# Kernel optimization log

Hardware: AMD Instinct MI355X
Metric: run time of the kernel (lower is better)

The kernel has to match this reference:

```python
import jax, jax.numpy as jnp
import numpy as np

N = 50000
E = 1600000
HID = 128
H = 8
D = HID // H


def _layer_norm(x, g, b, eps=1e-5):
    mu = jnp.mean(x, axis=-1, keepdims=True)
    var = jnp.mean(jnp.square(x - mu), axis=-1, keepdims=True)
    return (x - mu) * jax.lax.rsqrt(var + eps) * g + b


def setup_inputs() -> dict:
    key = jax.random.key(0)
    ks = jax.random.split(key, 20)
    s = 1.0 / np.sqrt(HID)
    inp = {
        "x": jax.random.normal(ks[0], (N, HID), jnp.float32),
        "edge_index": jax.random.randint(ks[1], (2, E), 0, N, jnp.int64),
        "edge_attr": jax.random.randint(ks[2], (E,), 0, 13, jnp.int64),
        # projections (stored as [in, out] so y = x @ W + b)
        "Wq": jax.random.normal(ks[3], (HID, HID), jnp.float32) * s,
        "bq": jnp.zeros((HID,), jnp.float32),
        "Wk": jax.random.normal(ks[4], (HID, HID), jnp.float32) * s,
        "bk": jnp.zeros((HID,), jnp.float32),
        "Wv": jax.random.normal(ks[5], (HID, HID), jnp.float32) * s,
        "bv": jnp.zeros((HID,), jnp.float32),
        "Wo": jax.random.normal(ks[6], (HID, HID), jnp.float32) * s,
        "bo": jnp.zeros((HID,), jnp.float32),
        "edge_bias_table": jax.random.normal(ks[7], (13, H), jnp.float32) * 0.02,
        "W1": jax.random.normal(ks[8], (HID, 4 * HID), jnp.float32) * s,
        "b1": jnp.zeros((4 * HID,), jnp.float32),
        "W2": jax.random.normal(ks[9], (4 * HID, HID), jnp.float32) * (0.5 * s),
        "b2": jnp.zeros((HID,), jnp.float32),
        "g1": jnp.ones((HID,), jnp.float32),
        "be1": jnp.zeros((HID,), jnp.float32),
        "g2": jnp.ones((HID,), jnp.float32),
        "be2": jnp.zeros((HID,), jnp.float32),
    }
    return inp


def reference(x, edge_index, edge_attr, Wq, bq, Wk, bk, Wv, bv, Wo, bo,
              edge_bias_table, W1, b1, W2, b2, g1, be1, g2, be2):
    n = x.shape[0]
    residual = x
    h = _layer_norm(x, g1, be1)
    Q = (h @ Wq + bq).reshape(n, H, D)
    K = (h @ Wk + bk).reshape(n, H, D)
    V = (h @ Wv + bv).reshape(n, H, D)
    src, dst = edge_index[0], edge_index[1]
    # per-edge scores [E, H]
    scores = jnp.sum(Q[dst] * K[src], axis=-1) / np.sqrt(D)
    scores = scores + edge_bias_table[jnp.clip(edge_attr, 0, 12)]
    # scatter softmax over incoming edges of each dst (global max, as in source)
    scores_exp = jnp.exp(scores - jnp.max(scores))
    attn_sum = jax.ops.segment_sum(scores_exp, dst, num_segments=n)  # [N, H]
    attn_w = scores_exp / (attn_sum[dst] + 1e-8)                      # [E, H]
    messages = V[src] * attn_w[..., None]                             # [E, H, D]
    out = jax.ops.segment_sum(messages, dst, num_segments=n)          # [N, H, D]
    out = out.reshape(n, HID) @ Wo + bo
    x = residual + out  # dropout is identity in eval
    residual = x
    h2 = _layer_norm(x, g2, be2)
    ffn = jax.nn.relu(h2 @ W1 + b1) @ W2 + b2
    return residual + ffn
```

## Files before the change

### kernel.cpp

```cpp
#include <hip/hip_runtime.h>
#include <hip/hip_bf16.h>

#define N_NODES 50000
#define E_EDGES 1600000
#define HID 128
#define NH 8
#define HD 16

#define NBKT 196
#define BKT_CAP 9216
#define CHUNK_A 4096
#define EPT 16
#define BINA_BLOCKS ((E_EDGES + CHUNK_A - 1) / CHUNK_A)
#define WCVT_BLOCKS 771
#define LN_BLOCKS 12500
#define QKV_XBLOCKS ((N_NODES + 127) / 128)
#define ATTN_BLOCKS 2048

using short8 = __attribute__((ext_vector_type(8))) short;
using f32x4  = __attribute__((ext_vector_type(4))) float;
using f32x2  = __attribute__((ext_vector_type(2))) float;
typedef _Float16 h16x2 __attribute__((ext_vector_type(2)));

#if defined(__has_builtin) && __has_builtin(__builtin_amdgcn_fdot2)
#define FDOT2(a, b, c) __builtin_amdgcn_fdot2((a), (b), (c), false)
#else
__device__ __forceinline__ float FDOT2(h16x2 a, h16x2 b, float c) {
    return fmaf((float)a[0], (float)b[0], fmaf((float)a[1], (float)b[1], c));
}
#endif

__device__ __forceinline__ float wave_reduce_sum(float v) {
    #pragma unroll
    for (int off = 32; off > 0; off >>= 1) v += __shfl_xor(v, off, 64);
    return v;
}

__device__ __forceinline__ unsigned int packbf2(float a, float b) {
    __hip_bfloat162 t;
    t.x = __float2bfloat16(a);
    t.y = __float2bfloat16(b);
    unsigned int u;
    __builtin_memcpy(&u, &t, 4);
    return u;
}

__device__ __forceinline__ unsigned short bf16u(float v) {
    __hip_bfloat16 t = __float2bfloat16(v);
    unsigned short u;
    __builtin_memcpy(&u, &t, 2);
    return u;
}

__device__ __forceinline__ unsigned char fp8e(float v) {
    return (unsigned char)(__builtin_amdgcn_cvt_pk_fp8_f32(v, v, 0u, false) & 0xFFu);
}

union U4H {
    uint4 u;
    h16x2 h[4];
};

struct KV {
    U4H k0, k1;
    uint4 v;
};

__device__ __forceinline__ KV loadkv(const char* khs, const unsigned char* v8s, unsigned pk) {
    KV r;
    unsigned rr = pk & 0xFFFFu;
    r.k0.u = *(const uint4*)(khs + (rr << 8));
    r.k1.u = *(const uint4*)(khs + (rr << 8) + 16u);
    r.v = *(const uint4*)(v8s + (rr << 7));
    return r;
}

__device__ __forceinline__ void consume_kv(const KV& kv, unsigned pk, bool vd,
                                           const U4H& q0, const U4H& q1,
                                           const float* bLDS, int sub,
                                           f32x2* acc2, float& wsum) {
    float p = 0.f;
    #pragma unroll
    for (int j = 0; j < 4; ++j) p = FDOT2(q0.h[j], kv.k0.h[j], p);
    #pragma unroll
    for (int j = 0; j < 4; ++j) p = FDOT2(q1.h[j], kv.k1.h[j], p);
    float s = p + bLDS[((pk >> 16) & 0xFu) * 8 + sub];
    float w = vd ? __expf(s) : 0.f;
    wsum += w;
    f32x2 w2; w2[0] = w; w2[1] = w;
    f32x2 t;
    t = __builtin_amdgcn_cvt_pk_f32_fp8(kv.v.x, false); acc2[0] = t * w2 + acc2[0];
    t = __builtin_amdgcn_cvt_pk_f32_fp8(kv.v.x, true);  acc2[1] = t * w2 + acc2[1];
    t = __builtin_amdgcn_cvt_pk_f32_fp8(kv.v.y, false); acc2[2] = t * w2 + acc2[2];
    t = __builtin_amdgcn_cvt_pk_f32_fp8(kv.v.y, true);  acc2[3] = t * w2 + acc2[3];
    t = __builtin_amdgcn_cvt_pk_f32_fp8(kv.v.z, false); acc2[4] = t * w2 + acc2[4];
    t = __builtin_amdgcn_cvt_pk_f32_fp8(kv.v.z, true);  acc2[5] = t * w2 + acc2[5];
    t = __builtin_amdgcn_cvt_pk_f32_fp8(kv.v.w, false); acc2[6] = t * w2 + acc2[6];
    t = __builtin_amdgcn_cvt_pk_f32_fp8(kv.v.w, true);  acc2[7] = t * w2 + acc2[7];
}

__global__ __launch_bounds__(256) void prep_kernel(
    const int* __restrict__ ei, const int* __restrict__ attr,
    int* __restrict__ bcur, unsigned int* __restrict__ temp,
    const float* __restrict__ Wq, const float* __restrict__ Wk,
    const float* __restrict__ Wv, const float* __restrict__ Wo,
    const float* __restrict__ W1, const float* __restrict__ W2,
    const float* __restrict__ bq, const float* __restrict__ bk,
    const float* __restrict__ bv,
    __hip_bfloat16* __restrict__ Wqkvt, __hip_bfloat16* __restrict__ Wot,
    __hip_bfloat16* __restrict__ W1t, __hip_bfloat16* __restrict__ W2t,
    float* __restrict__ bqkv,
    const float* __restrict__ x, const float* __restrict__ g1,
    const float* __restrict__ be1, __hip_bfloat16* __restrict__ h_out) {
    __shared__ unsigned int sval[CHUNK_A];
    __shared__ unsigned short sbkt[CHUNK_A];
    __shared__ int hist[NBKT];
    __shared__ int lofs[NBKT];
    __shared__ int gbase[NBKT];
    __shared__ int lcur[NBKT];
    __shared__ int sc[256];
    const int b = blockIdx.x;
    const int tid = threadIdx.x;
    if (b < BINA_BLOCKS) {
        const int e0 = b * CHUNK_A;
        const int n = min(CHUNK_A, E_EDGES - e0);
        for (int i = tid; i < NBKT; i += 256) hist[i] = 0;
        __syncthreads();
        unsigned int v[EPT];
        short bk_[EPT];
        #pragma unroll
        for (int j = 0; j < EPT; ++j) {
            int i = tid + j * 256;
            bk_[j] = -1;
            v[j] = 0;
            if (i < n) {
                int e = e0 + i;
                int src = ei[e];
                int dst = ei[E_EDGES + e];
                int a = attr[e]; a = min(max(a, 0), 12);
                v[j] = (unsigned)src | ((unsigned)a << 16) | ((unsigned)(dst & 255) << 20);
                int bb = dst >> 8;
                bk_[j] = (short)bb;
                atomicAdd(&hist[bb], 1);
            }
        }
        __syncthreads();
        sc[tid] = (tid < NBKT) ? hist[tid] : 0;
        __syncthreads();
        for (int off = 1; off < 256; off <<= 1) {
            int xx = (tid >= off) ? sc[tid - off] : 0;
            __syncthreads();
            sc[tid] += xx;
            __syncthreads();
        }
        if (tid < NBKT) {
            int h = hist[tid];
            lofs[tid] = sc[tid] - h;
            lcur[tid] = 0;
            gbase[tid] = h ? atomicAdd(&bcur[tid], h) : 0;
        }
        __syncthreads();
        #pragma unroll
        for (int j = 0; j < EPT; ++j) {
            if (bk_[j] >= 0) {
                int p = lofs[bk_[j]] + atomicAdd(&lcur[bk_[j]], 1);
                sval[p] = v[j];
                sbkt[p] = (unsigned short)bk_[j];
            }
        }
        __syncthreads();
        for (int i = tid; i < n; i += 256) {
            int bb = sbkt[i];
            temp[(size_t)bb * BKT_CAP + gbase[bb] + (i - lofs[bb])] = sval[i];
        }
    } else if (b < BINA_BLOCKS + WCVT_BLOCKS) {
        int t = (b - BINA_BLOCKS) * 256 + tid;
        if (t >= 196608) {
            int i = t - 196608;
            if (i < 384) bqkv[i] = i < 128 ? bq[i] : (i < 256 ? bk[i - 128] : bv[i - 256]);
            return;
        }
        const float* W; __hip_bfloat16* Wt; int K, N, idx;
        if (t < 65536) {
            int which = t >> 14; idx = t & 16383; K = 128; N = 128;
            W = which == 0 ? Wq : which == 1 ? Wk : which == 2 ? Wv : Wo;
            Wt = which == 3 ? Wot : Wqkvt + which * 16384;
        } else if (t < 131072) { idx = t - 65536;  K = 128; N = 512; W = W1; Wt = W1t; }
        else                   { idx = t - 131072; K = 512; N = 128; W = W2; Wt = W2t; }
        int n = idx / K, k = idx - n * K;
        Wt[idx] = __float2bfloat16(W[(size_t)k * N + n]);
    } else {
        int wave = tid >> 6;
        int lane = tid & 63;
        int row = (b - BINA_BLOCKS - WCVT_BLOCKS) * 4 + wave;
        if (row >= N_NODES) return;
        float2 v = ((const float2*)(x + (size_t)row * HID))[lane];
        float s = wave_reduce_sum(v.x + v.y);
        float mu = s * (1.0f / HID);
        float dx = v.x - mu, dy = v.y - mu;
        float q = wave_reduce_sum(dx * dx + dy * dy);
        float rstd = rsqrtf(q * (1.0f / HID) + 1e-5f);
        float2 gg = ((const float2*)g1)[lane];
        float2 bb = ((const float2*)be1)[lane];
        __hip_bfloat162 o;
        o.x = __float2bfloat16(dx * rstd * gg.x + bb.x);
        o.y = __float2bfloat16(dy * rstd * gg.y + bb.y);
        ((__hip_bfloat162*)(h_out + (size_t)row * HID))[lane] = o;
    }
}

__global__ __launch_bounds__(512) void qkv_binb_kernel(
    const int* __restrict__ bcur, const unsigned int* __restrict__ temp,
    unsigned int* __restrict__ packed, int* __restrict__ offs,
    const __hip_bfloat16* __restrict__ A, const __hip_bfloat16* __restrict__ Wt,
    const float* __restrict__ bias,
    _Float16* __restrict__ Chh, unsigned char* __restrict__ C8, int M) {
    __shared__ short8 smem[2048 + 2048];
    const int tid = threadIdx.x;
    if (blockIdx.x < NBKT) {
        int* cnts = (int*)smem;
        int* hist = cnts + 256;
        int* cur = hist + 256;
        const int b = blockIdx.x;
        if (tid < 256) {
            cnts[tid] = (tid < NBKT) ? bcur[tid] : 0;
            hist[tid] = 0;
        }
        __syncthreads();
        for (int off = 1; off < 256; off <<= 1) {
            int x = 0;
            if (tid < 256 && tid >= off) x = cnts[tid - off];
            __syncthreads();
            if (tid < 256) cnts[tid] += x;
            __syncthreads();
        }
        const int cnt = bcur[b];
        const int start = cnts[b] - cnt;
        const size_t base = (size_t)b * BKT_CAP;
        for (int i = tid; i < cnt; i += 512)
            atomicAdd(&hist[(temp[base + i] >> 20) & 255], 1);
        __syncthreads();
        if (tid < 256) cur[tid] = hist[tid];
        __syncthreads();
        for (int off = 1; off < 256; off <<= 1) {
            int x = 0;
            if (tid < 256 && tid >= off) x = cur[tid - off];
            __syncthreads();
            if (tid < 256) cur[tid] += x;
            __syncthreads();
        }
        const int node0 = b * 256;
        if (tid < 256) {
            int excl = cur[tid] - hist[tid];
            cur[tid] = excl;
            int node = node0 + tid;
            if (node < N_NODES) offs[node] = start + excl;
        }
        if (b == NBKT - 1 && tid == 0) offs[N_NODES] = start + cnt;
        __syncthreads();
        for (int i = tid; i < cnt; i += 512) {
            unsigned int v = temp[base + i];
            int d = (v >> 20) & 255;
            int p = start + atomicAdd(&cur[d], 1);
            packed[p] = v & 0xFFFFFu;
        }
        return;
    }
    const int gb = blockIdx.x - NBKT;
    const int plane = gb / QKV_XBLOCKS;
    const int xb = gb - plane * QKV_XBLOCKS;
    const int row0 = xb * 128;
    const int col0 = plane * 128;
    const int w = tid >> 6, l = tid & 63;
    const int lr = l & 15, hi = l >> 4;
    f32x4 acc[8] = {};
    #pragma unroll
    for (int it = 0; it < 4; ++it) {
        unsigned d = tid + it * 512;
        int r = d >> 4, sd = d & 15;
        int ss = sd ^ (r & 7);
        int gr = row0 + r; if (gr >= M) gr = M - 1;
        __builtin_amdgcn_global_load_lds(
            (const __attribute__((address_space(1))) void*)(A + (size_t)gr * 128 + ss * 8),
            (__attribute__((address_space(3))) void*)(smem + (d & ~63u)),
            16, 0, 0);
    }
    #pragma unroll
    for (int it = 0; it < 4; ++it) {
        unsigned d = tid + it * 512;
        int r = d >> 4, sd = d & 15;
        int ss = sd ^ (r & 7);
        __builtin_amdgcn_global_load_lds(
            (const __attribute__((address_space(1))) void*)(Wt + (size_t)(col0 + r) * 128 + ss * 8),
            (__attribute__((address_space(3))) void*)(smem + 2048 + (d & ~63u)),
            16, 0, 0);
    }
    __syncthreads();
    const int ar = w * 16 + lr;
    #pragma unroll
    for (int ks = 0; ks < 4; ++ks) {
        int s = ks * 4 + hi;
        short8 a = smem[ar * 16 + (s ^ (ar & 7))];
        #pragma unroll
        for (int f = 0; f < 8; ++f) {
            int br = f * 16 + lr;
            short8 b = smem[2048 + br * 16 + (s ^ (br & 7))];
            acc[f] = __builtin_amdgcn_mfma_f32_16x16x32_bf16(a, b, acc[f], 0, 0, 0);
        }
    }
    const float scl = (plane == 0) ? 0.25f : 1.0f;
    #pragma unroll
    for (int f = 0; f < 8; ++f) {
        int c = col0 + f * 16 + lr;
        float bv = bias[c];
        #pragma unroll
        for (int j = 0; j < 4; ++j) {
            int r = row0 + w * 16 + hi * 4 + j;
            if (r < M) {
                float v = acc[f][j] + bv;
                if (plane < 2)
                    Chh[(size_t)plane * N_NODES * 128 + (size_t)r * 128 + (c & 127)] =
                        (_Float16)(v * scl);
                else
                    C8[(size_t)r * 128 + (c & 127)] = fp8e(v);
            }
        }
    }
}

__global__ __launch_bounds__(256) void tail_kernel(
    const __hip_bfloat16* __restrict__ attn_ob,
    const __hip_bfloat16* __restrict__ Wot,
    const float* __restrict__ bo,
    const float* __restrict__ x,
    const float* __restrict__ g2, const float* __restrict__ be2,
    const __hip_bfloat16* __restrict__ W1t,
    const float* __restrict__ b1,
    const __hip_bfloat16* __restrict__ W2t,
    const float* __restrict__ b2,
    float* __restrict__ outp, int M) {
    __shared__ short8 hseg[32 * 16];
    __shared__ short8 wseg[2048];
    __shared__ short8 bseg[1024];
    __shared__ float lnS[2][32];
    __shared__ float lnQ[2][32];
    const int tid = threadIdx.x;
    const int row0 = blockIdx.x * 32;
    const int w = tid >> 6, l = tid & 63;
    const int lr = l & 15, hi = l >> 4;
    const int rt = w & 1, ch = w >> 1;
    #pragma unroll
    for (int it = 0; it < 2; ++it) {
        unsigned d = tid + it * 256;
        int r = d >> 4, sd = d & 15;
        int ss = sd ^ (r & 7);
        int gr = row0 + r; if (gr >= M) gr = M - 1;
        __builtin_amdgcn_global_load_lds(
            (const __attribute__((address_space(1))) void*)(attn_ob + (size_t)gr * 128 + ss * 8),
            (__attribute__((address_space(3))) void*)(hseg + (d & ~63u)),
            16, 0, 0);
    }
    #pragma unroll
    for (int it = 0; it < 8; ++it) {
        unsigned d = tid + it * 256;
        int r = d >> 4, sd = d & 15;
        int ss = sd ^ (r & 7);
        __builtin_amdgcn_global_load_lds(
            (const __attribute__((address_space(1))) void*)(Wot + (size_t)r * 128 + ss * 8),
            (__attribute__((address_space(3))) void*)(wseg + (d & ~63u)),
            16, 0, 0);
    }
    __syncthreads();
    const int ar = rt * 16 + lr;
    f32x4 acc[4] = {};
    #pragma unroll
    for (int ks = 0; ks < 4; ++ks) {
        int s = ks * 4 + hi;
        short8 a = hseg[ar * 16 + (s ^ (ar & 7))];
        #pragma unroll
        for (int f = 0; f < 4; ++f) {
            int br = ch * 64 + f * 16 + lr;
            short8 b = wseg[br * 16 + (s ^ (br & 7))];
            acc[f] = __builtin_amdgcn_mfma_f32_16x16x32_bf16(a, b, acc[f], 0, 0, 0);
        }
    }
    float vv[4][4];
    float gc[4], bc[4];
    #pragma unroll
    for (int f = 0; f < 4; ++f) {
        int c = ch * 64 + f * 16 + lr;
        gc[f] = g2[c]; bc[f] = be2[c];
        float bv = bo[c];
        #pragma unroll
        for (int j = 0; j < 4; ++j) {
            int r = row0 + rt * 16 + hi * 4 + j;
            int rr = r < M ? r : M - 1;
            vv[f][j] = acc[f][j] + bv + x[(size_t)rr * 128 + c];
        }
    }
    float ps[4], pq[4];
    #pragma unroll
    for (int j = 0; j < 4; ++j) {
        float s = 0.f, q = 0.f;
        #pragma unroll
        for (int f = 0; f < 4; ++f) { s += vv[f][j]; q += vv[f][j] * vv[f][j]; }
        #pragma unroll
        for (int m = 1; m <= 8; m <<= 1) { s += __shfl_xor(s, m); q += __shfl_xor(q, m); }
        ps[j] = s; pq[j] = q;
    }
    if (lr == 0) {
        #pragma unroll
        for (int j = 0; j < 4; ++j) {
            int r = rt * 16 + hi * 4 + j;
            lnS[ch][r] = ps[j];
            lnQ[ch][r] = pq[j];
        }
    }
    __syncthreads();
    unsigned short* hu = (unsigned short*)hseg;
    #pragma unroll
    for (int j = 0; j < 4; ++j) {
        int r = rt * 16 + hi * 4 + j;
        float s = lnS[0][r] + lnS[1][r];
        float q = lnQ[0][r] + lnQ[1][r];
        float mu = s * (1.0f / 128.0f);
        float rstd = rsqrtf(q * (1.0f / 128.0f) - mu * mu + 1e-5f);
        #pragma unroll
        for (int f = 0; f < 4; ++f) {
            int c = ch * 64 + f * 16 + lr;
            int seg = c >> 3;
            float hv = (vv[f][j] - mu) * rstd * gc[f] + bc[f];
            hu[r * 128 + ((seg ^ (r & 7)) << 3) + (c & 7)] = bf16u(hv);
        }
    }
    __syncthreads();
    unsigned short* f1u = (unsigned short*)wseg;
    for (int cc = 0; cc < 8; ++cc) {
        #pragma unroll
        for (int it = 0; it < 4; ++it) {
            unsigned d = tid + it * 256;
            int rb = d >> 4, sd = d & 15;
            int ss = sd ^ (rb & 7);
            __builtin_amdgcn_global_load_lds(
                (const __attribute__((address_space(1))) void*)(W1t + (size_t)(cc * 64 + rb) * 128 + ss * 8),
                (__attribute__((address_space(3))) void*)(bseg + (d & ~63u)),
                16, 0, 0);
        }
        __syncthreads();
        f32x4 a0 = {}, a1 = {};
        #pragma unroll
        for (int ks = 0; ks < 4; ++ks) {
            int s = ks * 4 + hi;
            short8 a = hseg[ar * 16 + (s ^ (ar & 7))];
            int rb0 = ch * 32 + lr;
            short8 b0 = bseg[rb0 * 16 + (s ^ (rb0 & 7))];
            a0 = __builtin_amdgcn_mfma_f32_16x16x32_bf16(a, b0, a0, 0, 0, 0);
            int rb1 = ch * 32 + 16 + lr;
            short8 b1v = bseg[rb1 * 16 + (s ^ (rb1 & 7))];
            a1 = __builtin_amdgcn_mfma_f32_16x16x32_bf16(a, b1v, a1, 0, 0, 0);
        }
        #pragma unroll
        for (int f = 0; f < 2; ++f) {
            int c = cc * 64 + ch * 32 + f * 16 + lr;
            float bv = b1[c];
            int seg = c >> 3;
            #pragma unroll
            for (int j = 0; j < 4; ++j) {
                int r = rt * 16 + hi * 4 + j;
                float v = fmaxf((f == 0 ? a0[j] : a1[j]) + bv, 0.f);
                f1u[r * 512 + ((seg ^ (r & 7)) << 3) + (c & 7)] = bf16u(v);
            }
        }
        __syncthreads();
    }
    f32x4 acc2[4] = {};
    for (int kc = 0; kc < 8; ++kc) {
        #pragma unroll
        for (int it = 0; it < 4; ++it) {
            unsigned d = tid + it * 256;
            int rb = d >> 3, sd = d & 7;
            int ss = sd ^ (rb & 7);
            __builtin_amdgcn_global_load_lds(
                (const __attribute__((address_space(1))) void*)(W2t + (size_t)rb * 512 + kc * 64 + ss * 8),
                (__attribute__((address_space(3))) void*)(bseg + (d & ~63u)),
                16, 0, 0);
        }
        __syncthreads();
        #pragma unroll
        for (int ks = 0; ks < 2; ++ks) {
            int ksg = kc * 8 + ks * 4 + hi;
            short8 a = *(const short8*)&f1u[ar * 512 + ((ksg ^ (ar & 7)) << 3)];
            int s2 = ks * 4 + hi;
            #pragma unroll
            for (int f = 0; f < 4; ++f) {
                int rb = ch * 64 + f * 16 + lr;
                short8 b = bseg[rb * 8 + (s2 ^ (rb & 7))];
                acc2[f] = __builtin_amdgcn_mfma_f32_16x16x32_bf16(a, b, acc2[f], 0, 0, 0);
            }
        }
        __syncthreads();
    }
    #pragma unroll
    for (int f = 0; f < 4; ++f) {
        int c = ch * 64 + f * 16 + lr;
        float bv = b2[c];
        #pragma unroll
        for (int j = 0; j < 4; ++j) {
            int r = row0 + rt * 16 + hi * 4 + j;
            if (r < M)
                outp[(size_t)r * 128 + c] = acc2[f][j] + bv + vv[f][j];
        }
    }
}

__global__ __launch_bounds__(256) void fused_attn_kernel(
    const unsigned int* __restrict__ packed,
    const int* __restrict__ offs,
    const _Float16* __restrict__ qkh,
    const unsigned char* __restrict__ v8p,
    const float* __restrict__ btab,
    __hip_bfloat16* __restrict__ out) {
    __shared__ float bLDS[104];
    const int tid = threadIdx.x;
    if (tid < 104) bLDS[tid] = btab[tid];
    __syncthreads();
    const int wave = tid >> 6, lane = tid & 63;
    const int slot = lane >> 3, sub = lane & 7;
    const char* qh = (const char*)qkh;
    const unsigned sb = (unsigned)sub << 5;
    const char* khs = (const char*)(qkh + (size_t)N_NODES * 128) + sb;
    const unsigned char* v8s = v8p + (sb >> 1);
    const unsigned gwave = blockIdx.x * 4 + wave;
    const unsigned stride = ATTN_BLOCKS * 4;
    for (unsigned n = gwave; n < N_NODES; n += stride) {
        U4H q0, q1;
        q0.u = *(const uint4*)(qh + (n << 8) + sb);
        q1.u = *(const uint4*)(qh + (n << 8) + sb + 16u);
        const int lo = offs[n], hi = offs[n + 1];
        const int nit = (hi - lo + 7) >> 3;
        f32x2 acc2[8] = {};
        float wsum = 0.f;
        int i = lo + slot;
        bool vd0 = i < hi;       unsigned pk0 = vd0 ? packed[i] : 0u;
        bool vd1 = i + 8 < hi;   unsigned pk1 = vd1 ? packed[i + 8] : 0u;
        KV a = loadkv(khs, v8s, pk0);
        KV b = loadkv(khs, v8s, pk1);
        int ii = i + 16;
        int rem = nit;
        while (rem >= 2) {
            const bool vd2 = ii < hi;
            const unsigned pk2 = vd2 ? packed[ii] : 0u;
            const bool vd3 = ii + 8 < hi;
            const unsigned pk3 = vd3 ? packed[ii + 8] : 0u;
            consume_kv(a, pk0, vd0, q0, q1, bLDS, sub, acc2, wsum);
            a = loadkv(khs, v8s, pk2);
            consume_kv(b, pk1, vd1, q0, q1, bLDS, sub, acc2, wsum);
            b = loadkv(khs, v8s, pk3);
            pk0 = pk2; vd0 = vd2;
            pk1 = pk3; vd1 = vd3;
            ii += 16;
            rem -= 2;
        }
        if (rem == 1) consume_kv(a, pk0, vd0, q0, q1, bLDS, sub, acc2, wsum);
        float accf[16];
        #pragma unroll
        for (int j = 0; j < 8; ++j) { accf[2 * j] = acc2[j][0]; accf[2 * j + 1] = acc2[j][1]; }
        #pragma unroll
        for (int j = 0; j < 16; ++j) {
            accf[j] += __shfl_xor(accf[j], 8);
            accf[j] += __shfl_xor(accf[j], 16);
            accf[j] += __shfl_xor(accf[j], 32);
        }
        wsum += __shfl_xor(wsum, 8);
        wsum += __shfl_xor(wsum, 16);
        wsum += __shfl_xor(wsum, 32);
        if (slot == 0) {
            float inv = 1.0f / (wsum + 1e-8f);
            uint4 o0, o1;
            o0.x = packbf2(accf[0] * inv, accf[1] * inv);
            o0.y = packbf2(accf[2] * inv, accf[3] * inv);
            o0.z = packbf2(accf[4] * inv, accf[5] * inv);
            o0.w = packbf2(accf[6] * inv, accf[7] * inv);
            o1.x = packbf2(accf[8] * inv, accf[9] * inv);
            o1.y = packbf2(accf[10] * inv, accf[11] * inv);
            o1.z = packbf2(accf[12] * inv, accf[13] * inv);
            o1.w = packbf2(accf[14] * inv, accf[15] * inv);
            char* op = (char*)out + (n << 8) + ((unsigned)sub << 5);
            *(uint4*)op = o0;
            *(uint4*)(op + 16) = o1;
        }
    }
}

extern "C" void kernel_launch(void* const* d_in, const int* in_sizes, int n_in,
                              void* d_out, int out_size, void* d_ws, size_t ws_size,
                              hipStream_t stream) {
    const float* x    = (const float*)d_in[0];
    const int*   ei   = (const int*)d_in[1];
    const int*   attr = (const int*)d_in[2];
    const float* Wq   = (const float*)d_in[3];
    const float* bq   = (const float*)d_in[4];
    const float* Wk   = (const float*)d_in[5];
    const float* bk   = (const float*)d_in[6];
    const float* Wv   = (const float*)d_in[7];
    const float* bv   = (const float*)d_in[8];
    const float* Wo   = (const float*)d_in[9];
    const float* bo   = (const float*)d_in[10];
    const float* ebt  = (const float*)d_in[11];
    const float* W1   = (const float*)d_in[12];
    const float* b1   = (const float*)d_in[13];
    const float* W2   = (const float*)d_in[14];
    const float* b2   = (const float*)d_in[15];
    const float* g1   = (const float*)d_in[16];
    const float* be1  = (const float*)d_in[17];
    const float* g2   = (const float*)d_in[18];
    const float* be2  = (const float*)d_in[19];
    float* out = (float*)d_out;

    char* ws = (char*)d_ws;
    const size_t szRowB = (size_t)N_NODES * HID * 2;
    const size_t ALIGN = 256;
    #define ALN(v) (((v) + ALIGN - 1) & ~(ALIGN - 1))
    size_t o = 0;
    __hip_bfloat16* h_buf = (__hip_bfloat16*)(ws + o); o += szRowB;
    _Float16* QKh = (_Float16*)(ws + o); o += (size_t)N_NODES * 256 * 2;
    unsigned char* V8 = (unsigned char*)(ws + o); o += (size_t)N_NODES * 128;
    unsigned int* packed = (unsigned int*)(ws + o); o += (size_t)E_EDGES * 4;
    unsigned int* temp = (unsigned int*)(ws + o); o += (size_t)NBKT * BKT_CAP * 4;
    int* bcur = (int*)(ws + o); o = ALN(o + (size_t)NBKT * 4);
    int* offs = (int*)(ws + o); o = ALN(o + (size_t)(N_NODES + 1) * 4);
    __hip_bfloat16* attn_ob = (__hip_bfloat16*)(ws + o); o += szRowB;
    __hip_bfloat16* Wqkvt = (__hip_bfloat16*)(ws + o); o += 384 * 128 * 2;
    __hip_bfloat16* Wot = (__hip_bfloat16*)(ws + o); o += 128 * 128 * 2;
    __hip_bfloat16* W1t = (__hip_bfloat16*)(ws + o); o += 512 * 128 * 2;
    __hip_bfloat16* W2t = (__hip_bfloat16*)(ws + o); o += 128 * 512 * 2;
    float* bqkv = (float*)(ws + o); o += 384 * 4;

    hipMemsetAsync(bcur, 0, (size_t)NBKT * 4, stream);

    prep_kernel<<<BINA_BLOCKS + WCVT_BLOCKS + LN_BLOCKS, 256, 0, stream>>>(
        ei, attr, bcur, temp,
        Wq, Wk, Wv, Wo, W1, W2, bq, bk, bv,
        Wqkvt, Wot, W1t, W2t, bqkv,
        x, g1, be1, h_buf);

    qkv_binb_kernel<<<NBKT + QKV_XBLOCKS * 3, 512, 0, stream>>>(
        bcur, temp, packed, offs,
        h_buf, Wqkvt, bqkv, QKh, V8, N_NODES);

    fused_attn_kernel<<<ATTN_BLOCKS, 256, 0, stream>>>(packed, offs, QKh, V8, ebt, attn_ob);

    tail_kernel<<<(N_NODES + 31) / 32, 256, 0, stream>>>(
        attn_ob, Wot, bo, x, g2, be2, W1t, b1, W2t, b2, out, N_NODES);
}
```

Measured before the change: 201.1 us.

## Double-buffer FFN weight tiles and edge-balance node ranges in attention

In the tail kernel, the W1 and W2 weight chunks are now double-buffered in LDS. The next chunk is prefetched with global_load_lds while the current one feeds the MFMAs, so one barrier per chunk is dropped. This doubles the bseg footprint, which can lower occupancy. The attention kernel also switches from a grid-stride node loop to contiguous node ranges per wave, chosen by binary search on the CSR offsets so each wave gets a roughly equal share of edges.

```diff
diff --git a/kernel.cpp b/kernel.cpp
--- a/kernel.cpp
+++ b/kernel.cpp
@@ -16,6 +16,7 @@
 #define LN_BLOCKS 12500
 #define QKV_XBLOCKS ((N_NODES + 127) / 128)
 #define ATTN_BLOCKS 2048
+#define ATTN_WAVES (ATTN_BLOCKS * 4)
 
 using short8 = __attribute__((ext_vector_type(8))) short;
 using f32x4  = __attribute__((ext_vector_type(4))) float;
@@ -341,7 +342,7 @@
     float* __restrict__ outp, int M) {
     __shared__ short8 hseg[32 * 16];
     __shared__ short8 wseg[2048];
-    __shared__ short8 bseg[1024];
+    __shared__ short8 bseg[2][1024];
     __shared__ float lnS[2][32];
     __shared__ float lnQ[2][32];
     const int tid = threadIdx.x;
@@ -370,6 +371,16 @@
             (__attribute__((address_space(3))) void*)(wseg + (d & ~63u)),
             16, 0, 0);
     }
+    #pragma unroll
+    for (int it = 0; it < 4; ++it) {
+        unsigned d = tid + it * 256;
+        int rb = d >> 4, sd = d & 15;
+        int ss = sd ^ (rb & 7);
+        __builtin_amdgcn_global_load_lds(
+            (const __attribute__((address_space(1))) void*)(W1t + (size_t)rb * 128 + ss * 8),
+            (__attribute__((address_space(3))) void*)(bseg[0] + (d & ~63u)),
+            16, 0, 0);
+    }
     __syncthreads();
     const int ar = rt * 16 + lr;
     f32x4 acc[4] = {};
@@ -436,27 +447,41 @@
     __syncthreads();
     unsigned short* f1u = (unsigned short*)wseg;
     for (int cc = 0; cc < 8; ++cc) {
-        #pragma unroll
-        for (int it = 0; it < 4; ++it) {
-            unsigned d = tid + it * 256;
-            int rb = d >> 4, sd = d & 15;
-            int ss = sd ^ (rb & 7);
-            __builtin_amdgcn_global_load_lds(
-                (const __attribute__((address_space(1))) void*)(W1t + (size_t)(cc * 64 + rb) * 128 + ss * 8),
-                (__attribute__((address_space(3))) void*)(bseg + (d & ~63u)),
-                16, 0, 0);
-        }
-        __syncthreads();
+        if (cc + 1 < 8) {
+            short8* dst = bseg[(cc + 1) & 1];
+            #pragma unroll
+            for (int it = 0; it < 4; ++it) {
+                unsigned d = tid + it * 256;
+                int rb = d >> 4, sd = d & 15;
+                int ss = sd ^ (rb & 7);
+                __builtin_amdgcn_global_load_lds(
+                    (const __attribute__((address_space(1))) void*)(W1t + (size_t)((cc + 1) * 64 + rb) * 128 + ss * 8),
+                    (__attribute__((address_space(3))) void*)(dst + (d & ~63u)),
+                    16, 0, 0);
+            }
+        } else {
+            #pragma unroll
+            for (int it = 0; it < 4; ++it) {
+                unsigned d = tid + it * 256;
+                int rb = d >> 3, sd = d & 7;
+                int ss = sd ^ (rb & 7);
+                __builtin_amdgcn_global_load_lds(
+                    (const __attribute__((address_space(1))) void*)(W2t + (size_t)rb * 512 + ss * 8),
+                    (__attribute__((address_space(3))) void*)(bseg[0] + (d & ~63u)),
+                    16, 0, 0);
+            }
+        }
+        const short8* cur = bseg[cc & 1];
         f32x4 a0 = {}, a1 = {};
         #pragma unroll
         for (int ks = 0; ks < 4; ++ks) {
             int s = ks * 4 + hi;
             short8 a = hseg[ar * 16 + (s ^ (ar & 7))];
             int rb0 = ch * 32 + lr;
-            short8 b0 = bseg[rb0 * 16 + (s ^ (rb0 & 7))];
+            short8 b0 = cur[rb0 * 16 + (s ^ (rb0 & 7))];
             a0 = __builtin_amdgcn_mfma_f32_16x16x32_bf16(a, b0, a0, 0, 0, 0);
             int rb1 = ch * 32 + 16 + lr;
-            short8 b1v = bseg[rb1 * 16 + (s ^ (rb1 & 7))];
+            short8 b1v = cur[rb1 * 16 + (s ^ (rb1 & 7))];
             a1 = __builtin_amdgcn_mfma_f32_16x16x32_bf16(a, b1v, a1, 0, 0, 0);
         }
         #pragma unroll
@@ -475,17 +500,20 @@
     }
     f32x4 acc2[4] = {};
     for (int kc = 0; kc < 8; ++kc) {
-        #pragma unroll
-        for (int it = 0; it < 4; ++it) {
-            unsigned d = tid + it * 256;
-            int rb = d >> 3, sd = d & 7;
-            int ss = sd ^ (rb & 7);
-            __builtin_amdgcn_global_load_lds(
-                (const __attribute__((address_space(1))) void*)(W2t + (size_t)rb * 512 + kc * 64 + ss * 8),
-                (__attribute__((address_space(3))) void*)(bseg + (d & ~63u)),
-                16, 0, 0);
-        }
-        __syncthreads();
+        if (kc + 1 < 8) {
+            short8* dst = bseg[(kc + 1) & 1];
+            #pragma unroll
+            for (int it = 0; it < 4; ++it) {
+                unsigned d = tid + it * 256;
+                int rb = d >> 3, sd = d & 7;
+                int ss = sd ^ (rb & 7);
+                __builtin_amdgcn_global_load_lds(
+                    (const __attribute__((address_space(1))) void*)(W2t + (size_t)rb * 512 + (kc + 1) * 64 + ss * 8),
+                    (__attribute__((address_space(3))) void*)(dst + (d & ~63u)),
+                    16, 0, 0);
+            }
+        }
+        const short8* cur = bseg[kc & 1];
         #pragma unroll
         for (int ks = 0; ks < 2; ++ks) {
             int ksg = kc * 8 + ks * 4 + hi;
@@ -494,7 +522,7 @@
             #pragma unroll
             for (int f = 0; f < 4; ++f) {
                 int rb = ch * 64 + f * 16 + lr;
-                short8 b = bseg[rb * 8 + (s2 ^ (rb & 7))];
+                short8 b = cur[rb * 8 + (s2 ^ (rb & 7))];
                 acc2[f] = __builtin_amdgcn_mfma_f32_16x16x32_bf16(a, b, acc2[f], 0, 0, 0);
             }
         }
@@ -530,12 +558,20 @@
     const unsigned sb = (unsigned)sub << 5;
     const char* khs = (const char*)(qkh + (size_t)N_NODES * 128) + sb;
     const unsigned char* v8s = v8p + (sb >> 1);
-    const unsigned gwave = blockIdx.x * 4 + wave;
-    const unsigned stride = ATTN_BLOCKS * 4;
-    for (unsigned n = gwave; n < N_NODES; n += stride) {
+    const unsigned wid = blockIdx.x * 4 + wave;
+    long long t0 = (long long)E_EDGES * wid / ATTN_WAVES;
+    long long t1 = (long long)E_EDGES * (wid + 1) / ATTN_WAVES;
+    int lo_ = 0, hi_ = N_NODES;
+    while (lo_ < hi_) { int mid = (lo_ + hi_) >> 1; if ((long long)offs[mid] < t0) lo_ = mid + 1; else hi_ = mid; }
+    const int n0 = lo_;
+    lo_ = n0; hi_ = N_NODES;
+    while (lo_ < hi_) { int mid = (lo_ + hi_) >> 1; if ((long long)offs[mid] < t1) lo_ = mid + 1; else hi_ = mid; }
+    int n1 = lo_;
+    if (wid == ATTN_WAVES - 1) n1 = N_NODES;
+    for (int n = n0; n < n1; ++n) {
         U4H q0, q1;
-        q0.u = *(const uint4*)(qh + (n << 8) + sb);
-        q1.u = *(const uint4*)(qh + (n << 8) + sb + 16u);
+        q0.u = *(const uint4*)(qh + ((unsigned)n << 8) + sb);
+        q1.u = *(const uint4*)(qh + ((unsigned)n << 8) + sb + 16u);
         const int lo = offs[n], hi = offs[n + 1];
         const int nit = (hi - lo + 7) >> 3;
         f32x2 acc2[8] = {};
@@ -585,7 +621,7 @@
             o1.y = packbf2(accf[10] * inv, accf[11] * inv);
             o1.z = packbf2(accf[12] * inv, accf[13] * inv);
             o1.w = packbf2(accf[14] * inv, accf[15] * inv);
-            char* op = (char*)out + (n << 8) + ((unsigned)sub << 5);
+            char* op = (char*)out + ((unsigned)n << 8) + ((unsigned)sub << 5);
             *(uint4*)op = o0;
             *(uint4*)(op + 16) = o1;
         }
```

Result: slower. 210.7 us (+4.7%).
